# Optimization experiments

Measured on AMD Instinct MI355X. Metric: run time of the kernel, lower is better.

The kernel has to match this reference:

```python
import jax, jax.numpy as jnp
import numpy as np

B, V, S, H, I, L, NH = 32, 50, 64, 256, 512, 2, 4
VOCAB, SEGV, AGEV = 30000, 2, 144
EPS = 1e-12


def _ln(x, g, b):
    m = jnp.mean(x, axis=-1, keepdims=True)
    v = jnp.mean((x - m) ** 2, axis=-1, keepdims=True)
    return (x - m) / jnp.sqrt(v + EPS) * g + b


def _sinusoid_table(max_pos, hidden):
    pos = np.arange(max_pos, dtype=np.float32)[:, None]
    idx = np.arange(hidden, dtype=np.float32)[None, :]
    ang = pos / np.power(10000.0, 2.0 * idx / hidden)
    tab = np.where((np.arange(hidden) % 2 == 0)[None, :], np.sin(ang), np.cos(ang))
    return jnp.asarray(tab, dtype=jnp.float32)


def setup_inputs() -> dict:
    key = jax.random.key(0)
    ks = iter(jax.random.split(key, 48))

    def nrm(shape, s=0.02):
        return jax.random.normal(next(ks), shape, dtype=jnp.float32) * s

    inp = {
        "word": jax.random.randint(next(ks), (B, V, S), 0, VOCAB),
        "age": jax.random.randint(next(ks), (B, V, S), 0, AGEV),
        "seg": jax.random.randint(next(ks), (B, V, S), 0, SEGV),
        "posi": jax.random.randint(next(ks), (B, V, S), 0, S),
        "mask": jnp.ones((B, V, S), dtype=jnp.float32),
        "token": 0,
        "word_emb": nrm((VOCAB, H)),
        "seg_emb": nrm((SEGV, H)),
        "age_emb": nrm((AGEV, H)),
        "posi_emb": _sinusoid_table(S, H),
        "emb_ln_g": jnp.ones((H,), jnp.float32),
        "emb_ln_b": jnp.zeros((H,), jnp.float32),
        "qw": nrm((L, H, H)), "qb": jnp.zeros((L, H), jnp.float32),
        "kw": nrm((L, H, H)), "kb": jnp.zeros((L, H), jnp.float32),
        "vw": nrm((L, H, H)), "vb": jnp.zeros((L, H), jnp.float32),
        "ow": nrm((L, H, H)), "ob": jnp.zeros((L, H), jnp.float32),
        "attn_ln_g": jnp.ones((L, H), jnp.float32),
        "attn_ln_b": jnp.zeros((L, H), jnp.float32),
        "iw": nrm((L, H, I)), "ib": jnp.zeros((L, I), jnp.float32),
        "outw": nrm((L, I, H)), "outb": jnp.zeros((L, H), jnp.float32),
        "out_ln_g": jnp.ones((L, H), jnp.float32),
        "out_ln_b": jnp.zeros((L, H), jnp.float32),
        "pool_w": nrm((H, H)), "pool_b": jnp.zeros((H,), jnp.float32),
    }
    return inp


def reference(word, age, seg, posi, mask, token,
              word_emb, seg_emb, age_emb, posi_emb, emb_ln_g, emb_ln_b,
              qw, qb, kw, kb, vw, vb, ow, ob, attn_ln_g, attn_ln_b,
              iw, ib, outw, outb, out_ln_g, out_ln_b, pool_w, pool_b):
    # token embeddings: word + seg + age + sinusoidal position, then LayerNorm
    emb = word_emb[word] + seg_emb[seg] + age_emb[age] + posi_emb[posi]  # [B,V,S,H]
    x = _ln(emb, emb_ln_g, emb_ln_b)
    N = B * V
    x = x.reshape(N, S, H)  # vectorize the per-visit loop over the batch axis
    am = ((1.0 - mask) * -10000.0).reshape(N, 1, 1, S)  # additive attention mask
    d = H // NH
    scale = 1.0 / jnp.sqrt(jnp.float32(d))
    n_layers = qw.shape[0]
    for l in range(n_layers):
        q = (x @ qw[l] + qb[l]).reshape(N, S, NH, d)
        k = (x @ kw[l] + kb[l]).reshape(N, S, NH, d)
        v = (x @ vw[l] + vb[l]).reshape(N, S, NH, d)
        scores = jnp.einsum("bqhd,bkhd->bhqk", q, k) * scale + am
        probs = jax.nn.softmax(scores, axis=-1)  # dropout = identity (eval)
        ctx = jnp.einsum("bhqk,bkhd->bqhd", probs, v).reshape(N, S, H)
        a = _ln(ctx @ ow[l] + ob[l] + x, attn_ln_g[l], attn_ln_b[l])
        h = jax.nn.gelu(a @ iw[l] + ib[l], approximate=False)
        x = _ln(h @ outw[l] + outb[l] + a, out_ln_g[l], out_ln_b[l])
    first = x[:, 0].reshape(B, V, H)  # pooler with token=False: hidden[:, 0]
    return jnp.tanh(first @ pool_w + pool_b)  # [B, V, H]
```

## Files before the change

### kernel.cpp

```cpp
#include <hip/hip_runtime.h>
#include <math.h>

typedef __attribute__((ext_vector_type(8))) short short8;
typedef __attribute__((ext_vector_type(4))) short short4v;
typedef __attribute__((ext_vector_type(4))) float f32x4;

#define M_TOT 102400

__device__ __forceinline__ unsigned short f2b(float f) {
  unsigned u = __float_as_uint(f);
  return (unsigned short)((u + 0x7fffu + ((u >> 16) & 1u)) >> 16);
}
__device__ __forceinline__ float b2f(unsigned short h) {
  return __uint_as_float(((unsigned)h) << 16);
}
__device__ __forceinline__ f32x4 mfma16(short8 a, short8 b, f32x4 c) {
  return __builtin_amdgcn_mfma_f32_16x16x32_bf16(a, b, c, 0, 0, 0);
}
template <int STRIDE>
__device__ __forceinline__ short8 lds8(const short* buf, int row, int k) {
  int idx = (row * STRIDE + k) ^ ((row & 7) << 3);
  return *(const short8*)(buf + idx);
}
template <int STRIDE>
__device__ __forceinline__ void ldsw(short* buf, int row, int col, unsigned short v) {
  buf[(row * STRIDE + col) ^ ((row & 7) << 3)] = (short)v;
}
__device__ __forceinline__ float red16sum(float v) {
  v += __shfl_xor(v, 1); v += __shfl_xor(v, 2);
  v += __shfl_xor(v, 4); v += __shfl_xor(v, 8);
  return v;
}
__device__ __forceinline__ float red16max(float v) {
  v = fmaxf(v, __shfl_xor(v, 1)); v = fmaxf(v, __shfl_xor(v, 2));
  v = fmaxf(v, __shfl_xor(v, 4)); v = fmaxf(v, __shfl_xor(v, 8));
  return v;
}

__device__ __forceinline__ void stage16k(const short* __restrict__ g, short* l,
                                         int w, int lane) {
  const char* gb = (const char*)g + w * 4096 + lane * 16;
  char* lb = (char*)l + w * 4096;
#pragma unroll
  for (int c = 0; c < 4; ++c)
    __builtin_amdgcn_global_load_lds(
        (const __attribute__((address_space(1))) unsigned int*)(gb + c * 1024),
        (__attribute__((address_space(3))) unsigned int*)(lb + c * 1024), 16, 0, 0);
}

template <int KB>
__device__ __forceinline__ void gemm_core(const short* __restrict__ A, int lda,
                                          const short* __restrict__ Wimg,
                                          short* sB, f32x4 acc[16], int r0,
                                          int w, int lane, int l15, int g4) {
  short8 af[KB];
#pragma unroll
  for (int kk = 0; kk < KB; ++kk)
    af[kk] = *(const short8*)(A + (r0 + l15) * lda + kk * 32 + g4 * 8);
  stage16k(Wimg, sB, w, lane);
  __syncthreads();
#pragma unroll
  for (int kb = 0; kb < KB; ++kb) {
    if (kb + 1 < KB)
      stage16k(Wimg + (kb + 1) * 8192, sB + ((kb + 1) & 1) * 8192, w, lane);
    const short* cur = sB + (kb & 1) * 8192;
#pragma unroll
    for (int tc = 0; tc < 16; ++tc) {
      int row = tc * 16 + l15;
      short8 bf = *(const short8*)(cur + ((row * 32 + g4 * 8) ^ ((row & 7) << 3)));
      acc[tc] = mfma16(af[kb], bf, acc[tc]);
    }
    __syncthreads();
  }
}

__device__ __forceinline__ void ln_epi(f32x4 acc[16], short* x,
                                       const float* __restrict__ bias,
                                       const float* __restrict__ g_,
                                       const float* __restrict__ b_,
                                       int r0, int l15, int g4) {
  float s1[4] = {0.f, 0.f, 0.f, 0.f}, s2[4] = {0.f, 0.f, 0.f, 0.f};
#pragma unroll
  for (int tc = 0; tc < 16; ++tc) {
    int col = tc * 16 + l15;
    float bv = bias[col];
#pragma unroll
    for (int r = 0; r < 4; ++r) {
      float v = acc[tc][r] + bv + b2f((unsigned short)x[(r0 + g4 * 4 + r) * 256 + col]);
      acc[tc][r] = v;
      s1[r] += v; s2[r] += v * v;
    }
  }
  float mean[4], rstd[4];
#pragma unroll
  for (int r = 0; r < 4; ++r) {
    float a = red16sum(s1[r]), q = red16sum(s2[r]);
    mean[r] = a * (1.f / 256.f);
    rstd[r] = rsqrtf(q * (1.f / 256.f) - mean[r] * mean[r] + 1e-12f);
  }
#pragma unroll
  for (int tc = 0; tc < 16; ++tc) {
    int col = tc * 16 + l15;
    float gv = g_[col], bv = b_[col];
#pragma unroll
    for (int r = 0; r < 4; ++r)
      x[(r0 + g4 * 4 + r) * 256 + col] =
          (short)f2b((acc[tc][r] - mean[r]) * rstd[r] * gv + bv);
  }
}

__global__ void prep_w(const float* __restrict__ qw, const float* __restrict__ kw,
                       const float* __restrict__ vw, const float* __restrict__ ow,
                       const float* __restrict__ iw, const float* __restrict__ outw,
                       const float* __restrict__ pw, short* __restrict__ ws) {
  int t = blockIdx.x * 256 + threadIdx.x;
  float val; int base, n, k;
  if (t < 524288) {
    int which = t >> 17, r = t & 131071;
    int ly = r >> 16, e = r & 65535;
    n = e >> 8; k = e & 255;
    const float* m = which == 0 ? qw : which == 1 ? kw : which == 2 ? vw : ow;
    val = m[(ly * 256 + k) * 256 + n];
    base = which * 131072 + ly * 65536;
  } else if (t < 786432) {
    int e = t - 524288;
    int ly = e >> 17, f = e & 131071, g2 = f >> 16, e2 = f & 65535;
    n = e2 >> 8; k = e2 & 255;
    val = iw[(ly * 256 + k) * 512 + g2 * 256 + n];
    base = 524288 + ly * 131072 + g2 * 65536;
  } else if (t < 1048576) {
    int e = t - 786432;
    int ly = e >> 17, f = e & 131071;
    n = f >> 9; k = f & 511;
    val = outw[(ly * 512 + k) * 256 + n];
    base = 786432 + ly * 131072;
  } else {
    int e = t - 1048576;
    n = e >> 8; k = e & 255;
    val = pw[k * 256 + n];
    base = 1048576;
  }
  int pos = ((n * 32 + (k & 31)) ^ ((n & 7) << 3));
  ws[base + (k >> 5) * 8192 + pos] = (short)f2b(val);
}

__global__ __launch_bounds__(256) void emb_k(
    const int* __restrict__ word, const int* __restrict__ age,
    const int* __restrict__ seg, const int* __restrict__ posi,
    const float* __restrict__ we, const float* __restrict__ se,
    const float* __restrict__ ae, const float* __restrict__ pe,
    const float* __restrict__ g, const float* __restrict__ b,
    short* __restrict__ x) {
  int w = threadIdx.x >> 6, lane = threadIdx.x & 63;
  int t = blockIdx.x * 4 + w;
  int wi = word[t], gi = seg[t], ai = age[t], pi = posi[t];
  f32x4 e = ((const f32x4*)(we + wi * 256))[lane];
  f32x4 tv = ((const f32x4*)(se + gi * 256))[lane]; e = e + tv;
  tv = ((const f32x4*)(ae + ai * 256))[lane]; e = e + tv;
  tv = ((const f32x4*)(pe + pi * 256))[lane]; e = e + tv;
  float s1 = e[0] + e[1] + e[2] + e[3];
  float s2 = e[0] * e[0] + e[1] * e[1] + e[2] * e[2] + e[3] * e[3];
#pragma unroll
  for (int m = 1; m < 64; m <<= 1) { s1 += __shfl_xor(s1, m); s2 += __shfl_xor(s2, m); }
  float mean = s1 * (1.f / 256.f);
  float rstd = rsqrtf(s2 * (1.f / 256.f) - mean * mean + 1e-12f);
  f32x4 gv = ((const f32x4*)g)[lane];
  f32x4 bv = ((const f32x4*)b)[lane];
  short4v pk;
#pragma unroll
  for (int j = 0; j < 4; ++j) pk[j] = (short)f2b((e[j] - mean) * rstd * gv[j] + bv[j]);
  *(short4v*)(x + t * 256 + lane * 4) = pk;
}

__global__ __launch_bounds__(256) void qkv3_k(
    const short* __restrict__ x, const short* __restrict__ img,
    const float* __restrict__ qb_, const float* __restrict__ kb_,
    const float* __restrict__ vb_,
    short* __restrict__ q, short* __restrict__ k2, short* __restrict__ vt, int ly) {
  __shared__ __align__(16) short sB[16384];
  int w = threadIdx.x >> 6, lane = threadIdx.x & 63;
  int l15 = lane & 15, g4 = lane >> 4;
  int y = blockIdx.y;
  int r0 = blockIdx.x * 64 + w * 16;
  const short* W = img + y * 131072 + ly * 65536;
  const float* bias = (y == 0 ? qb_ : y == 1 ? kb_ : vb_) + ly * 256;
  f32x4 acc[16];
#pragma unroll
  for (int i = 0; i < 16; ++i) acc[i] = f32x4{0.f, 0.f, 0.f, 0.f};
  gemm_core<8>(x, 256, W, sB, acc, r0, w, lane, l15, g4);
  if (y < 2) {
    short* out = y ? k2 : q;
#pragma unroll
    for (int tc = 0; tc < 16; ++tc) {
      int col = tc * 16 + l15;
      float bv = bias[col];
#pragma unroll
      for (int r = 0; r < 4; ++r)
        out[(r0 + g4 * 4 + r) * 256 + col] = (short)f2b(acc[tc][r] + bv);
    }
  } else {
#pragma unroll
    for (int tc = 0; tc < 16; ++tc) {
      int col = tc * 16 + l15;
      float bv = bias[col];
#pragma unroll
      for (int r = 0; r < 4; ++r) {
        int tok = r0 + g4 * 4 + r;
        vt[(tok >> 6) * 16384 + col * 64 + (tok & 63)] = (short)f2b(acc[tc][r] + bv);
      }
    }
  }
}

__global__ __launch_bounds__(256) void attn_k(
    const short* __restrict__ q, const short* __restrict__ k,
    const short* __restrict__ vt, short* __restrict__ ctx,
    const float* __restrict__ mask) {
  __shared__ __align__(16) short sP[16384];
  int w = threadIdx.x >> 6, lane = threadIdx.x & 63;
  int l15 = lane & 15, g4 = lane >> 4;
  int n = blockIdx.x;
  const f32x4 zero4 = {0.f, 0.f, 0.f, 0.f};
  short* sPw = sP + w * 4096;

  float amvr[4];
#pragma unroll
  for (int tc = 0; tc < 4; ++tc)
    amvr[tc] = (1.f - mask[n * 64 + tc * 16 + l15]) * -10000.f;

  const short* qn = q + n * 16384;
  const short* kn = k + n * 16384;
  const short* vtn = vt + n * 16384;

  short8 qa[4][2];
#pragma unroll
  for (int st = 0; st < 4; ++st)
#pragma unroll
    for (int ks = 0; ks < 2; ++ks)
      qa[st][ks] = *(const short8*)(qn + (st * 16 + l15) * 256 + w * 64 + ks * 32 + g4 * 8);
  f32x4 sacc[4][4];
#pragma unroll
  for (int st = 0; st < 4; ++st)
#pragma unroll
    for (int tc = 0; tc < 4; ++tc) sacc[st][tc] = zero4;
#pragma unroll
  for (int ks = 0; ks < 2; ++ks)
#pragma unroll
    for (int tc = 0; tc < 4; ++tc) {
      short8 kf = *(const short8*)(kn + (tc * 16 + l15) * 256 + w * 64 + ks * 32 + g4 * 8);
#pragma unroll
      for (int st = 0; st < 4; ++st) sacc[st][tc] = mfma16(qa[st][ks], kf, sacc[st][tc]);
    }
#pragma unroll
  for (int st = 0; st < 4; ++st)
#pragma unroll
    for (int r = 0; r < 4; ++r) {
      float pv[4];
      float mx = -1e30f;
#pragma unroll
      for (int tc = 0; tc < 4; ++tc) {
        float sv = sacc[st][tc][r] * 0.125f + amvr[tc];
        pv[tc] = sv;
        mx = fmaxf(mx, sv);
      }
      mx = red16max(mx);
      float sm = 0.f;
#pragma unroll
      for (int tc = 0; tc < 4; ++tc) {
        float e = __expf(pv[tc] - mx);
        pv[tc] = e;
        sm += e;
      }
      sm = red16sum(sm);
      float inv = 1.f / sm;
#pragma unroll
      for (int tc = 0; tc < 4; ++tc)
        ldsw<64>(sPw, st * 16 + g4 * 4 + r, tc * 16 + l15, f2b(pv[tc] * inv));
    }
  __syncthreads();

  f32x4 cacc[4][4];
#pragma unroll
  for (int st = 0; st < 4; ++st)
#pragma unroll
    for (int tc = 0; tc < 4; ++tc) cacc[st][tc] = zero4;
#pragma unroll
  for (int ks = 0; ks < 2; ++ks) {
    short8 pa[4];
#pragma unroll
    for (int st = 0; st < 4; ++st) pa[st] = lds8<64>(sPw, st * 16 + l15, ks * 32 + g4 * 8);
#pragma unroll
    for (int tc = 0; tc < 4; ++tc) {
      short8 vf = *(const short8*)(vtn + (w * 64 + tc * 16 + l15) * 64 + ks * 32 + g4 * 8);
#pragma unroll
      for (int st = 0; st < 4; ++st) cacc[st][tc] = mfma16(pa[st], vf, cacc[st][tc]);
    }
  }
#pragma unroll
  for (int st = 0; st < 4; ++st)
#pragma unroll
    for (int tc = 0; tc < 4; ++tc)
#pragma unroll
      for (int r = 0; r < 4; ++r)
        ctx[(n * 64 + st * 16 + g4 * 4 + r) * 256 + w * 64 + tc * 16 + l15] =
            (short)f2b(cacc[st][tc][r]);
}

__global__ __launch_bounds__(256) void oln_k(
    const short* __restrict__ ctx, const short* __restrict__ img,
    const float* __restrict__ bias, short* __restrict__ x,
    const float* __restrict__ g_, const float* __restrict__ b_) {
  __shared__ __align__(16) short sB[16384];
  int w = threadIdx.x >> 6, lane = threadIdx.x & 63;
  int l15 = lane & 15, g4 = lane >> 4;
  int r0 = blockIdx.x * 64 + w * 16;
  f32x4 acc[16];
#pragma unroll
  for (int i = 0; i < 16; ++i) acc[i] = f32x4{0.f, 0.f, 0.f, 0.f};
  gemm_core<8>(ctx, 256, img, sB, acc, r0, w, lane, l15, g4);
  ln_epi(acc, x, bias, g_, b_, r0, l15, g4);
}

__global__ __launch_bounds__(256) void ffn1_k(
    const short* __restrict__ x, const short* __restrict__ img,
    const float* __restrict__ bias, short* __restrict__ h) {
  __shared__ __align__(16) short sB[16384];
  int w = threadIdx.x >> 6, lane = threadIdx.x & 63;
  int l15 = lane & 15, g4 = lane >> 4;
  int y = blockIdx.y;
  int r0 = blockIdx.x * 64 + w * 16;
  f32x4 acc[16];
#pragma unroll
  for (int i = 0; i < 16; ++i) acc[i] = f32x4{0.f, 0.f, 0.f, 0.f};
  gemm_core<8>(x, 256, img + y * 65536, sB, acc, r0, w, lane, l15, g4);
  const float* bs = bias + y * 256;
#pragma unroll
  for (int tc = 0; tc < 16; ++tc) {
    int col = tc * 16 + l15;
    float bv = bs[col];
#pragma unroll
    for (int r = 0; r < 4; ++r) {
      float v = acc[tc][r] + bv;
      v = 0.5f * v * (1.f + erff(v * 0.70710678118f));
      h[(r0 + g4 * 4 + r) * 512 + y * 256 + col] = (short)f2b(v);
    }
  }
}

__global__ __launch_bounds__(256) void ffn2_k(
    const short* __restrict__ h, const short* __restrict__ img,
    const float* __restrict__ bias, short* __restrict__ x,
    const float* __restrict__ g_, const float* __restrict__ b_) {
  __shared__ __align__(16) short sB[16384];
  int w = threadIdx.x >> 6, lane = threadIdx.x & 63;
  int l15 = lane & 15, g4 = lane >> 4;
  int r0 = blockIdx.x * 64 + w * 16;
  f32x4 acc[16];
#pragma unroll
  for (int i = 0; i < 16; ++i) acc[i] = f32x4{0.f, 0.f, 0.f, 0.f};
  gemm_core<16>(h, 512, img, sB, acc, r0, w, lane, l15, g4);
  ln_epi(acc, x, bias, g_, b_, r0, l15, g4);
}

__global__ __launch_bounds__(256) void pool_k(
    const short* __restrict__ x, const short* __restrict__ img,
    const float* __restrict__ pb, float* __restrict__ out) {
  __shared__ __align__(16) short sB[16384];
  int w = threadIdx.x >> 6, lane = threadIdx.x & 63;
  int l15 = lane & 15, g4 = lane >> 4;
  int r0 = blockIdx.x * 64 + w * 16;
  f32x4 acc[16];
#pragma unroll
  for (int i = 0; i < 16; ++i) acc[i] = f32x4{0.f, 0.f, 0.f, 0.f};
  gemm_core<8>(x, 16384, img, sB, acc, r0, w, lane, l15, g4);
#pragma unroll
  for (int tc = 0; tc < 16; ++tc) {
    int col = tc * 16 + l15;
    float bv = pb[col];
#pragma unroll
    for (int r = 0; r < 4; ++r)
      out[(r0 + g4 * 4 + r) * 256 + col] = tanhf(acc[tc][r] + bv);
  }
}

extern "C" void kernel_launch(void* const* d_in, const int* in_sizes, int n_in,
                              void* d_out, int out_size, void* d_ws, size_t ws_size,
                              hipStream_t stream) {
  const int* word = (const int*)d_in[0];
  const int* age = (const int*)d_in[1];
  const int* seg = (const int*)d_in[2];
  const int* posi = (const int*)d_in[3];
  const float* mask = (const float*)d_in[4];
  const float* word_emb = (const float*)d_in[6];
  const float* seg_emb = (const float*)d_in[7];
  const float* age_emb = (const float*)d_in[8];
  const float* posi_emb = (const float*)d_in[9];
  const float* emb_g = (const float*)d_in[10];
  const float* emb_b = (const float*)d_in[11];
  const float* qw = (const float*)d_in[12];
  const float* qb = (const float*)d_in[13];
  const float* kw = (const float*)d_in[14];
  const float* kb = (const float*)d_in[15];
  const float* vw = (const float*)d_in[16];
  const float* vb = (const float*)d_in[17];
  const float* ow = (const float*)d_in[18];
  const float* ob = (const float*)d_in[19];
  const float* attn_g = (const float*)d_in[20];
  const float* attn_b = (const float*)d_in[21];
  const float* iw = (const float*)d_in[22];
  const float* ib = (const float*)d_in[23];
  const float* outw = (const float*)d_in[24];
  const float* outb = (const float*)d_in[25];
  const float* out_g = (const float*)d_in[26];
  const float* out_b = (const float*)d_in[27];
  const float* pool_w = (const float*)d_in[28];
  const float* pool_b = (const float*)d_in[29];
  short* ws = (short*)d_ws;

  short* xb_ = ws + 1114112;
  short* qbuf = xb_ + 26214400;
  short* kbuf = qbuf + 26214400;
  short* vtbuf = kbuf + 26214400;
  short* hbuf = qbuf;

  prep_w<<<4352, 256, 0, stream>>>(qw, kw, vw, ow, iw, outw, pool_w, ws);
  emb_k<<<25600, 256, 0, stream>>>(word, age, seg, posi, word_emb, seg_emb,
                                   age_emb, posi_emb, emb_g, emb_b, xb_);
  for (int ly = 0; ly < 2; ++ly) {
    qkv3_k<<<dim3(1600, 3), 256, 0, stream>>>(xb_, ws, qb, kb, vb, qbuf, kbuf,
                                              vtbuf, ly);
    attn_k<<<1600, 256, 0, stream>>>(qbuf, kbuf, vtbuf, qbuf, mask);
    oln_k<<<1600, 256, 0, stream>>>(qbuf, ws + 393216 + ly * 65536, ob + ly * 256,
                                    xb_, attn_g + ly * 256, attn_b + ly * 256);
    ffn1_k<<<dim3(1600, 2), 256, 0, stream>>>(xb_, ws + 524288 + ly * 131072,
                                              ib + ly * 512, hbuf);
    ffn2_k<<<1600, 256, 0, stream>>>(hbuf, ws + 786432 + ly * 131072,
                                     outb + ly * 256, xb_, out_g + ly * 256,
                                     out_b + ly * 256);
  }
  pool_k<<<25, 256, 0, stream>>>(xb_, ws + 1048576, pool_b, (float*)d_out);
}
```

Measured before the change: 709.3 us.

## Fuse attention with output projection and retile GEMMs to 64x64 per wave

Each GEMM is retiled so every wave owns 64 output columns across all 64 rows, instead of 16 rows across all 256 columns. A-fragments are loaded once per block and reused across the Q/K/V and FFN1 output tiles, which replaces the extra grid dimension. The attention kernel now keeps the context in LDS and runs the output projection plus residual LayerNorm directly, so the ctx round-trip through global memory and one launch go away. The LayerNorm reduction now needs a cross-wave LDS partial-sum step with an extra barrier, and the larger af register arrays raise register pressure and may lower occupancy.

After: 1.186 ms. 67.2% more time.

```diff
diff --git a/kernel.cpp b/kernel.cpp
--- a/kernel.cpp
+++ b/kernel.cpp
@@ -4,8 +4,6 @@
 typedef __attribute__((ext_vector_type(8))) short short8;
 typedef __attribute__((ext_vector_type(4))) short short4v;
 typedef __attribute__((ext_vector_type(4))) float f32x4;
-
-#define M_TOT 102400
 
 __device__ __forceinline__ unsigned short f2b(float f) {
   unsigned u = __float_as_uint(f);
@@ -49,14 +47,10 @@
 }
 
 template <int KB>
-__device__ __forceinline__ void gemm_core(const short* __restrict__ A, int lda,
-                                          const short* __restrict__ Wimg,
-                                          short* sB, f32x4 acc[16], int r0,
-                                          int w, int lane, int l15, int g4) {
-  short8 af[KB];
-#pragma unroll
-  for (int kk = 0; kk < KB; ++kk)
-    af[kk] = *(const short8*)(A + (r0 + l15) * lda + kk * 32 + g4 * 8);
+__device__ __forceinline__ void gemm64(const short8 af[][4],
+                                       const short* __restrict__ Wimg,
+                                       short* sB, f32x4 acc[4][4],
+                                       int w, int lane, int l15, int g4) {
   stage16k(Wimg, sB, w, lane);
   __syncthreads();
 #pragma unroll
@@ -65,47 +59,74 @@
       stage16k(Wimg + (kb + 1) * 8192, sB + ((kb + 1) & 1) * 8192, w, lane);
     const short* cur = sB + (kb & 1) * 8192;
 #pragma unroll
-    for (int tc = 0; tc < 16; ++tc) {
-      int row = tc * 16 + l15;
-      short8 bf = *(const short8*)(cur + ((row * 32 + g4 * 8) ^ ((row & 7) << 3)));
-      acc[tc] = mfma16(af[kb], bf, acc[tc]);
+    for (int tc = 0; tc < 4; ++tc) {
+      int n = w * 64 + tc * 16 + l15;
+      short8 bf = *(const short8*)(cur + ((n * 32 + g4 * 8) ^ ((n & 7) << 3)));
+#pragma unroll
+      for (int st = 0; st < 4; ++st)
+        acc[st][tc] = mfma16(af[kb][st], bf, acc[st][tc]);
     }
     __syncthreads();
   }
 }
 
-__device__ __forceinline__ void ln_epi(f32x4 acc[16], short* x,
-                                       const float* __restrict__ bias,
-                                       const float* __restrict__ g_,
-                                       const float* __restrict__ b_,
-                                       int r0, int l15, int g4) {
-  float s1[4] = {0.f, 0.f, 0.f, 0.f}, s2[4] = {0.f, 0.f, 0.f, 0.f};
-#pragma unroll
-  for (int tc = 0; tc < 16; ++tc) {
-    int col = tc * 16 + l15;
+__device__ __forceinline__ void ln_epi64(f32x4 acc[4][4], short* x,
+                                         const float* __restrict__ bias,
+                                         const float* __restrict__ g_,
+                                         const float* __restrict__ b_,
+                                         float (*part)[64][4],
+                                         int r0, int w, int l15, int g4) {
+  float s1[4][4], s2[4][4];
+#pragma unroll
+  for (int st = 0; st < 4; ++st)
+#pragma unroll
+    for (int r = 0; r < 4; ++r) { s1[st][r] = 0.f; s2[st][r] = 0.f; }
+#pragma unroll
+  for (int tc = 0; tc < 4; ++tc) {
+    int col = w * 64 + tc * 16 + l15;
     float bv = bias[col];
 #pragma unroll
+    for (int st = 0; st < 4; ++st)
+#pragma unroll
+      for (int r = 0; r < 4; ++r) {
+        float v = acc[st][tc][r] + bv +
+                  b2f((unsigned short)x[(r0 + st * 16 + g4 * 4 + r) * 256 + col]);
+        acc[st][tc][r] = v;
+        s1[st][r] += v; s2[st][r] += v * v;
+      }
+  }
+#pragma unroll
+  for (int st = 0; st < 4; ++st)
+#pragma unroll
     for (int r = 0; r < 4; ++r) {
-      float v = acc[tc][r] + bv + b2f((unsigned short)x[(r0 + g4 * 4 + r) * 256 + col]);
-      acc[tc][r] = v;
-      s1[r] += v; s2[r] += v * v;
-    }
-  }
-  float mean[4], rstd[4];
-#pragma unroll
-  for (int r = 0; r < 4; ++r) {
-    float a = red16sum(s1[r]), q = red16sum(s2[r]);
-    mean[r] = a * (1.f / 256.f);
-    rstd[r] = rsqrtf(q * (1.f / 256.f) - mean[r] * mean[r] + 1e-12f);
-  }
-#pragma unroll
-  for (int tc = 0; tc < 16; ++tc) {
-    int col = tc * 16 + l15;
+      float a = red16sum(s1[st][r]), q = red16sum(s2[st][r]);
+      if (l15 == 0) {
+        part[0][st * 16 + g4 * 4 + r][w] = a;
+        part[1][st * 16 + g4 * 4 + r][w] = q;
+      }
+    }
+  __syncthreads();
+#pragma unroll
+  for (int st = 0; st < 4; ++st)
+#pragma unroll
+    for (int r = 0; r < 4; ++r) {
+      int row = st * 16 + g4 * 4 + r;
+      float a = part[0][row][0] + part[0][row][1] + part[0][row][2] + part[0][row][3];
+      float q = part[1][row][0] + part[1][row][1] + part[1][row][2] + part[1][row][3];
+      float mean = a * (1.f / 256.f);
+      float rstd = rsqrtf(q * (1.f / 256.f) - mean * mean + 1e-12f);
+      s1[st][r] = mean; s2[st][r] = rstd;
+    }
+#pragma unroll
+  for (int tc = 0; tc < 4; ++tc) {
+    int col = w * 64 + tc * 16 + l15;
     float gv = g_[col], bv = b_[col];
 #pragma unroll
-    for (int r = 0; r < 4; ++r)
-      x[(r0 + g4 * 4 + r) * 256 + col] =
-          (short)f2b((acc[tc][r] - mean[r]) * rstd[r] * gv + bv);
+    for (int st = 0; st < 4; ++st)
+#pragma unroll
+      for (int r = 0; r < 4; ++r)
+        x[(r0 + st * 16 + g4 * 4 + r) * 256 + col] =
+            (short)f2b((acc[st][tc][r] - s1[st][r]) * s2[st][r] * gv + bv);
   }
 }
 
@@ -172,7 +193,7 @@
   *(short4v*)(x + t * 256 + lane * 4) = pk;
 }
 
-__global__ __launch_bounds__(256) void qkv3_k(
+__global__ __launch_bounds__(256) void qkv_k(
     const short* __restrict__ x, const short* __restrict__ img,
     const float* __restrict__ qb_, const float* __restrict__ kb_,
     const float* __restrict__ vb_,
@@ -180,48 +201,64 @@
   __shared__ __align__(16) short sB[16384];
   int w = threadIdx.x >> 6, lane = threadIdx.x & 63;
   int l15 = lane & 15, g4 = lane >> 4;
-  int y = blockIdx.y;
-  int r0 = blockIdx.x * 64 + w * 16;
-  const short* W = img + y * 131072 + ly * 65536;
-  const float* bias = (y == 0 ? qb_ : y == 1 ? kb_ : vb_) + ly * 256;
-  f32x4 acc[16];
-#pragma unroll
-  for (int i = 0; i < 16; ++i) acc[i] = f32x4{0.f, 0.f, 0.f, 0.f};
-  gemm_core<8>(x, 256, W, sB, acc, r0, w, lane, l15, g4);
-  if (y < 2) {
-    short* out = y ? k2 : q;
-#pragma unroll
-    for (int tc = 0; tc < 16; ++tc) {
-      int col = tc * 16 + l15;
-      float bv = bias[col];
-#pragma unroll
-      for (int r = 0; r < 4; ++r)
-        out[(r0 + g4 * 4 + r) * 256 + col] = (short)f2b(acc[tc][r] + bv);
-    }
-  } else {
-#pragma unroll
-    for (int tc = 0; tc < 16; ++tc) {
-      int col = tc * 16 + l15;
-      float bv = bias[col];
-#pragma unroll
-      for (int r = 0; r < 4; ++r) {
-        int tok = r0 + g4 * 4 + r;
-        vt[(tok >> 6) * 16384 + col * 64 + (tok & 63)] = (short)f2b(acc[tc][r] + bv);
+  int n = blockIdx.x;
+  int r0 = n * 64;
+  short8 af[8][4];
+#pragma unroll
+  for (int kk = 0; kk < 8; ++kk)
+#pragma unroll
+    for (int st = 0; st < 4; ++st)
+      af[kk][st] = *(const short8*)(x + (r0 + st * 16 + l15) * 256 + kk * 32 + g4 * 8);
+
+  for (int y = 0; y < 3; ++y) {
+    f32x4 acc[4][4];
+#pragma unroll
+    for (int st = 0; st < 4; ++st)
+#pragma unroll
+      for (int tc = 0; tc < 4; ++tc) acc[st][tc] = f32x4{0.f, 0.f, 0.f, 0.f};
+    gemm64<8>(af, img + y * 131072 + ly * 65536, sB, acc, w, lane, l15, g4);
+    const float* bias = (y == 0 ? qb_ : y == 1 ? kb_ : vb_) + ly * 256;
+    if (y < 2) {
+      short* out = y ? k2 : q;
+#pragma unroll
+      for (int tc = 0; tc < 4; ++tc) {
+        int col = w * 64 + tc * 16 + l15;
+        float bv = bias[col];
+#pragma unroll
+        for (int st = 0; st < 4; ++st)
+#pragma unroll
+          for (int r = 0; r < 4; ++r)
+            out[(r0 + st * 16 + g4 * 4 + r) * 256 + col] = (short)f2b(acc[st][tc][r] + bv);
       }
-    }
-  }
-}
-
-__global__ __launch_bounds__(256) void attn_k(
+    } else {
+#pragma unroll
+      for (int tc = 0; tc < 4; ++tc) {
+        int col = w * 64 + tc * 16 + l15;
+        float bv = bias[col];
+#pragma unroll
+        for (int st = 0; st < 4; ++st)
+#pragma unroll
+          for (int r = 0; r < 4; ++r)
+            vt[n * 16384 + col * 64 + st * 16 + g4 * 4 + r] = (short)f2b(acc[st][tc][r] + bv);
+      }
+    }
+  }
+}
+
+__global__ __launch_bounds__(256) void attnoln_k(
     const short* __restrict__ q, const short* __restrict__ k,
-    const short* __restrict__ vt, short* __restrict__ ctx,
+    const short* __restrict__ vt, const short* __restrict__ img,
+    const float* __restrict__ ob_, short* __restrict__ x,
+    const float* __restrict__ g_, const float* __restrict__ b_,
     const float* __restrict__ mask) {
-  __shared__ __align__(16) short sP[16384];
+  __shared__ __align__(16) short sCtx[16384];
+  __shared__ __align__(16) short sPB[16384];
+  __shared__ float part[2][64][4];
   int w = threadIdx.x >> 6, lane = threadIdx.x & 63;
   int l15 = lane & 15, g4 = lane >> 4;
   int n = blockIdx.x;
   const f32x4 zero4 = {0.f, 0.f, 0.f, 0.f};
-  short* sPw = sP + w * 4096;
+  short* sPw = sPB + w * 4096;
 
   float amvr[4];
 #pragma unroll
@@ -302,23 +339,23 @@
     for (int tc = 0; tc < 4; ++tc)
 #pragma unroll
       for (int r = 0; r < 4; ++r)
-        ctx[(n * 64 + st * 16 + g4 * 4 + r) * 256 + w * 64 + tc * 16 + l15] =
-            (short)f2b(cacc[st][tc][r]);
-}
-
-__global__ __launch_bounds__(256) void oln_k(
-    const short* __restrict__ ctx, const short* __restrict__ img,
-    const float* __restrict__ bias, short* __restrict__ x,
-    const float* __restrict__ g_, const float* __restrict__ b_) {
-  __shared__ __align__(16) short sB[16384];
-  int w = threadIdx.x >> 6, lane = threadIdx.x & 63;
-  int l15 = lane & 15, g4 = lane >> 4;
-  int r0 = blockIdx.x * 64 + w * 16;
-  f32x4 acc[16];
-#pragma unroll
-  for (int i = 0; i < 16; ++i) acc[i] = f32x4{0.f, 0.f, 0.f, 0.f};
-  gemm_core<8>(ctx, 256, img, sB, acc, r0, w, lane, l15, g4);
-  ln_epi(acc, x, bias, g_, b_, r0, l15, g4);
+        ldsw<256>(sCtx, st * 16 + g4 * 4 + r, w * 64 + tc * 16 + l15,
+                  f2b(cacc[st][tc][r]));
+  __syncthreads();
+
+  short8 af[8][4];
+#pragma unroll
+  for (int kk = 0; kk < 8; ++kk)
+#pragma unroll
+    for (int st = 0; st < 4; ++st)
+      af[kk][st] = lds8<256>(sCtx, st * 16 + l15, kk * 32 + g4 * 8);
+  f32x4 acc[4][4];
+#pragma unroll
+  for (int st = 0; st < 4; ++st)
+#pragma unroll
+    for (int tc = 0; tc < 4; ++tc) acc[st][tc] = zero4;
+  gemm64<8>(af, img, sPB, acc, w, lane, l15, g4);
+  ln_epi64(acc, x, ob_, g_, b_, part, n * 64, w, l15, g4);
 }
 
 __global__ __launch_bounds__(256) void ffn1_k(
@@ -327,22 +364,33 @@
   __shared__ __align__(16) short sB[16384];
   int w = threadIdx.x >> 6, lane = threadIdx.x & 63;
   int l15 = lane & 15, g4 = lane >> 4;
-  int y = blockIdx.y;
-  int r0 = blockIdx.x * 64 + w * 16;
-  f32x4 acc[16];
-#pragma unroll
-  for (int i = 0; i < 16; ++i) acc[i] = f32x4{0.f, 0.f, 0.f, 0.f};
-  gemm_core<8>(x, 256, img + y * 65536, sB, acc, r0, w, lane, l15, g4);
-  const float* bs = bias + y * 256;
-#pragma unroll
-  for (int tc = 0; tc < 16; ++tc) {
-    int col = tc * 16 + l15;
-    float bv = bs[col];
-#pragma unroll
-    for (int r = 0; r < 4; ++r) {
-      float v = acc[tc][r] + bv;
-      v = 0.5f * v * (1.f + erff(v * 0.70710678118f));
-      h[(r0 + g4 * 4 + r) * 512 + y * 256 + col] = (short)f2b(v);
+  int r0 = blockIdx.x * 64;
+  short8 af[8][4];
+#pragma unroll
+  for (int kk = 0; kk < 8; ++kk)
+#pragma unroll
+    for (int st = 0; st < 4; ++st)
+      af[kk][st] = *(const short8*)(x + (r0 + st * 16 + l15) * 256 + kk * 32 + g4 * 8);
+  for (int p = 0; p < 2; ++p) {
+    f32x4 acc[4][4];
+#pragma unroll
+    for (int st = 0; st < 4; ++st)
+#pragma unroll
+      for (int tc = 0; tc < 4; ++tc) acc[st][tc] = f32x4{0.f, 0.f, 0.f, 0.f};
+    gemm64<8>(af, img + p * 65536, sB, acc, w, lane, l15, g4);
+    const float* bs = bias + p * 256;
+#pragma unroll
+    for (int tc = 0; tc < 4; ++tc) {
+      int col = w * 64 + tc * 16 + l15;
+      float bv = bs[col];
+#pragma unroll
+      for (int st = 0; st < 4; ++st)
+#pragma unroll
+        for (int r = 0; r < 4; ++r) {
+          float v = acc[st][tc][r] + bv;
+          v = 0.5f * v * (1.f + erff(v * 0.70710678118f));
+          h[(r0 + st * 16 + g4 * 4 + r) * 512 + p * 256 + col] = (short)f2b(v);
+        }
     }
   }
 }
@@ -352,14 +400,26 @@
     const float* __restrict__ bias, short* __restrict__ x,
     const float* __restrict__ g_, const float* __restrict__ b_) {
   __shared__ __align__(16) short sB[16384];
+  __shared__ float part[2][64][4];
   int w = threadIdx.x >> 6, lane = threadIdx.x & 63;
   int l15 = lane & 15, g4 = lane >> 4;
-  int r0 = blockIdx.x * 64 + w * 16;
-  f32x4 acc[16];
-#pragma unroll
-  for (int i = 0; i < 16; ++i) acc[i] = f32x4{0.f, 0.f, 0.f, 0.f};
-  gemm_core<16>(h, 512, img, sB, acc, r0, w, lane, l15, g4);
-  ln_epi(acc, x, bias, g_, b_, r0, l15, g4);
+  int r0 = blockIdx.x * 64;
+  f32x4 acc[4][4];
+#pragma unroll
+  for (int st = 0; st < 4; ++st)
+#pragma unroll
+    for (int tc = 0; tc < 4; ++tc) acc[st][tc] = f32x4{0.f, 0.f, 0.f, 0.f};
+  for (int half = 0; half < 2; ++half) {
+    short8 af[8][4];
+#pragma unroll
+    for (int kk = 0; kk < 8; ++kk)
+#pragma unroll
+      for (int st = 0; st < 4; ++st)
+        af[kk][st] = *(const short8*)(h + (r0 + st * 16 + l15) * 512 + half * 256 +
+                                      kk * 32 + g4 * 8);
+    gemm64<8>(af, img + half * 65536, sB, acc, w, lane, l15, g4);
+  }
+  ln_epi64(acc, x, bias, g_, b_, part, r0, w, l15, g4);
 }
 
 __global__ __launch_bounds__(256) void pool_k(
@@ -368,18 +428,29 @@
   __shared__ __align__(16) short sB[16384];
   int w = threadIdx.x >> 6, lane = threadIdx.x & 63;
   int l15 = lane & 15, g4 = lane >> 4;
-  int r0 = blockIdx.x * 64 + w * 16;
-  f32x4 acc[16];
-#pragma unroll
-  for (int i = 0; i < 16; ++i) acc[i] = f32x4{0.f, 0.f, 0.f, 0.f};
-  gemm_core<8>(x, 16384, img, sB, acc, r0, w, lane, l15, g4);
-#pragma unroll
-  for (int tc = 0; tc < 16; ++tc) {
-    int col = tc * 16 + l15;
+  int r0 = blockIdx.x * 64;
+  short8 af[8][4];
+#pragma unroll
+  for (int kk = 0; kk < 8; ++kk)
+#pragma unroll
+    for (int st = 0; st < 4; ++st)
+      af[kk][st] = *(const short8*)(x + (size_t)(r0 + st * 16 + l15) * 16384 +
+                                    kk * 32 + g4 * 8);
+  f32x4 acc[4][4];
+#pragma unroll
+  for (int st = 0; st < 4; ++st)
+#pragma unroll
+    for (int tc = 0; tc < 4; ++tc) acc[st][tc] = f32x4{0.f, 0.f, 0.f, 0.f};
+  gemm64<8>(af, img, sB, acc, w, lane, l15, g4);
+#pragma unroll
+  for (int tc = 0; tc < 4; ++tc) {
+    int col = w * 64 + tc * 16 + l15;
     float bv = pb[col];
 #pragma unroll
-    for (int r = 0; r < 4; ++r)
-      out[(r0 + g4 * 4 + r) * 256 + col] = tanhf(acc[tc][r] + bv);
+    for (int st = 0; st < 4; ++st)
+#pragma unroll
+      for (int r = 0; r < 4; ++r)
+        out[(r0 + st * 16 + g4 * 4 + r) * 256 + col] = tanhf(acc[st][tc][r] + bv);
   }
 }
 
@@ -427,13 +498,12 @@
   emb_k<<<25600, 256, 0, stream>>>(word, age, seg, posi, word_emb, seg_emb,
                                    age_emb, posi_emb, emb_g, emb_b, xb_);
   for (int ly = 0; ly < 2; ++ly) {
-    qkv3_k<<<dim3(1600, 3), 256, 0, stream>>>(xb_, ws, qb, kb, vb, qbuf, kbuf,
-                                              vtbuf, ly);
-    attn_k<<<1600, 256, 0, stream>>>(qbuf, kbuf, vtbuf, qbuf, mask);
-    oln_k<<<1600, 256, 0, stream>>>(qbuf, ws + 393216 + ly * 65536, ob + ly * 256,
-                                    xb_, attn_g + ly * 256, attn_b + ly * 256);
-    ffn1_k<<<dim3(1600, 2), 256, 0, stream>>>(xb_, ws + 524288 + ly * 131072,
-                                              ib + ly * 512, hbuf);
+    qkv_k<<<1600, 256, 0, stream>>>(xb_, ws, qb, kb, vb, qbuf, kbuf, vtbuf, ly);
+    attnoln_k<<<1600, 256, 0, stream>>>(qbuf, kbuf, vtbuf, ws + 393216 + ly * 65536,
+                                        ob + ly * 256, xb_, attn_g + ly * 256,
+                                        attn_b + ly * 256, mask);
+    ffn1_k<<<1600, 256, 0, stream>>>(xb_, ws + 524288 + ly * 131072, ib + ly * 512,
+                                     hbuf);
     ffn2_k<<<1600, 256, 0, stream>>>(hbuf, ws + 786432 + ly * 131072,
                                      outb + ly * 256, xb_, out_g + ly * 256,
                                      out_b + ly * 256);
```

## Retile GEMM warps to 2x2 layout and use tanh-approx GELU

Applied to the files above, without the earlier changes.

Each warp now computes a 32x128 output tile, so every LDS B fragment is reused across two row subtiles. This halves the LDS reads per MFMA compared with the old 16x256 per-warp tile. LayerNorm epilogues now reduce row statistics across two warps through a shared partial-sum buffer and an extra barrier. FFN2 is split into two K halves to bound register use. GELU switches from erf to a sigmoid-form tanh approximation with a fast exp, which trades some accuracy for fewer instructions.

After: 903.6 us. 27.4% more time.

```diff
diff --git a/kernel.cpp b/kernel.cpp
--- a/kernel.cpp
+++ b/kernel.cpp
@@ -4,8 +4,6 @@
 typedef __attribute__((ext_vector_type(8))) short short8;
 typedef __attribute__((ext_vector_type(4))) short short4v;
 typedef __attribute__((ext_vector_type(4))) float f32x4;
-
-#define M_TOT 102400
 
 __device__ __forceinline__ unsigned short f2b(float f) {
   unsigned u = __float_as_uint(f);
@@ -49,14 +47,10 @@
 }
 
 template <int KB>
-__device__ __forceinline__ void gemm_core(const short* __restrict__ A, int lda,
+__device__ __forceinline__ void gemm_core(const short8 af[][2],
                                           const short* __restrict__ Wimg,
-                                          short* sB, f32x4 acc[16], int r0,
+                                          short* sB, f32x4 acc[2][8],
                                           int w, int lane, int l15, int g4) {
-  short8 af[KB];
-#pragma unroll
-  for (int kk = 0; kk < KB; ++kk)
-    af[kk] = *(const short8*)(A + (r0 + l15) * lda + kk * 32 + g4 * 8);
   stage16k(Wimg, sB, w, lane);
   __syncthreads();
 #pragma unroll
@@ -65,47 +59,75 @@
       stage16k(Wimg + (kb + 1) * 8192, sB + ((kb + 1) & 1) * 8192, w, lane);
     const short* cur = sB + (kb & 1) * 8192;
 #pragma unroll
-    for (int tc = 0; tc < 16; ++tc) {
-      int row = tc * 16 + l15;
-      short8 bf = *(const short8*)(cur + ((row * 32 + g4 * 8) ^ ((row & 7) << 3)));
-      acc[tc] = mfma16(af[kb], bf, acc[tc]);
+    for (int tc = 0; tc < 8; ++tc) {
+      int n = (w & 1) * 128 + tc * 16 + l15;
+      short8 bf = *(const short8*)(cur + ((n * 32 + g4 * 8) ^ ((n & 7) << 3)));
+#pragma unroll
+      for (int st = 0; st < 2; ++st)
+        acc[st][tc] = mfma16(af[kb][st], bf, acc[st][tc]);
     }
     __syncthreads();
   }
 }
 
-__device__ __forceinline__ void ln_epi(f32x4 acc[16], short* x,
+__device__ __forceinline__ void ln_epi(f32x4 acc[2][8], short* x,
                                        const float* __restrict__ bias,
                                        const float* __restrict__ g_,
                                        const float* __restrict__ b_,
-                                       int r0, int l15, int g4) {
-  float s1[4] = {0.f, 0.f, 0.f, 0.f}, s2[4] = {0.f, 0.f, 0.f, 0.f};
-#pragma unroll
-  for (int tc = 0; tc < 16; ++tc) {
-    int col = tc * 16 + l15;
+                                       float (*part)[64][2],
+                                       int r0, int wr, int wc, int w,
+                                       int l15, int g4) {
+  float s1[2][4], s2[2][4];
+#pragma unroll
+  for (int st = 0; st < 2; ++st)
+#pragma unroll
+    for (int r = 0; r < 4; ++r) { s1[st][r] = 0.f; s2[st][r] = 0.f; }
+#pragma unroll
+  for (int tc = 0; tc < 8; ++tc) {
+    int col = wc + tc * 16 + l15;
     float bv = bias[col];
 #pragma unroll
+    for (int st = 0; st < 2; ++st)
+#pragma unroll
+      for (int r = 0; r < 4; ++r) {
+        float v = acc[st][tc][r] + bv +
+                  b2f((unsigned short)x[(r0 + wr + st * 16 + g4 * 4 + r) * 256 + col]);
+        acc[st][tc][r] = v;
+        s1[st][r] += v; s2[st][r] += v * v;
+      }
+  }
+#pragma unroll
+  for (int st = 0; st < 2; ++st)
+#pragma unroll
     for (int r = 0; r < 4; ++r) {
-      float v = acc[tc][r] + bv + b2f((unsigned short)x[(r0 + g4 * 4 + r) * 256 + col]);
-      acc[tc][r] = v;
-      s1[r] += v; s2[r] += v * v;
-    }
-  }
-  float mean[4], rstd[4];
-#pragma unroll
-  for (int r = 0; r < 4; ++r) {
-    float a = red16sum(s1[r]), q = red16sum(s2[r]);
-    mean[r] = a * (1.f / 256.f);
-    rstd[r] = rsqrtf(q * (1.f / 256.f) - mean[r] * mean[r] + 1e-12f);
-  }
-#pragma unroll
-  for (int tc = 0; tc < 16; ++tc) {
-    int col = tc * 16 + l15;
+      float a = red16sum(s1[st][r]), q = red16sum(s2[st][r]);
+      if (l15 == 0) {
+        part[0][wr + st * 16 + g4 * 4 + r][w & 1] = a;
+        part[1][wr + st * 16 + g4 * 4 + r][w & 1] = q;
+      }
+    }
+  __syncthreads();
+#pragma unroll
+  for (int st = 0; st < 2; ++st)
+#pragma unroll
+    for (int r = 0; r < 4; ++r) {
+      int row = wr + st * 16 + g4 * 4 + r;
+      float a = part[0][row][0] + part[0][row][1];
+      float q = part[1][row][0] + part[1][row][1];
+      float mean = a * (1.f / 256.f);
+      float rstd = rsqrtf(q * (1.f / 256.f) - mean * mean + 1e-12f);
+      s1[st][r] = mean; s2[st][r] = rstd;
+    }
+#pragma unroll
+  for (int tc = 0; tc < 8; ++tc) {
+    int col = wc + tc * 16 + l15;
     float gv = g_[col], bv = b_[col];
 #pragma unroll
-    for (int r = 0; r < 4; ++r)
-      x[(r0 + g4 * 4 + r) * 256 + col] =
-          (short)f2b((acc[tc][r] - mean[r]) * rstd[r] * gv + bv);
+    for (int st = 0; st < 2; ++st)
+#pragma unroll
+      for (int r = 0; r < 4; ++r)
+        x[(r0 + wr + st * 16 + g4 * 4 + r) * 256 + col] =
+            (short)f2b((acc[st][tc][r] - s1[st][r]) * s2[st][r] * gv + bv);
   }
 }
 
@@ -180,34 +202,48 @@
   __shared__ __align__(16) short sB[16384];
   int w = threadIdx.x >> 6, lane = threadIdx.x & 63;
   int l15 = lane & 15, g4 = lane >> 4;
+  int wr = (w >> 1) * 32, wc = (w & 1) * 128;
   int y = blockIdx.y;
-  int r0 = blockIdx.x * 64 + w * 16;
+  int n = blockIdx.x;
+  int r0 = n * 64;
   const short* W = img + y * 131072 + ly * 65536;
   const float* bias = (y == 0 ? qb_ : y == 1 ? kb_ : vb_) + ly * 256;
-  f32x4 acc[16];
-#pragma unroll
-  for (int i = 0; i < 16; ++i) acc[i] = f32x4{0.f, 0.f, 0.f, 0.f};
-  gemm_core<8>(x, 256, W, sB, acc, r0, w, lane, l15, g4);
+  short8 af[8][2];
+#pragma unroll
+  for (int kk = 0; kk < 8; ++kk)
+#pragma unroll
+    for (int st = 0; st < 2; ++st)
+      af[kk][st] = *(const short8*)(x + (r0 + wr + st * 16 + l15) * 256 + kk * 32 + g4 * 8);
+  f32x4 acc[2][8];
+#pragma unroll
+  for (int st = 0; st < 2; ++st)
+#pragma unroll
+    for (int tc = 0; tc < 8; ++tc) acc[st][tc] = f32x4{0.f, 0.f, 0.f, 0.f};
+  gemm_core<8>(af, W, sB, acc, w, lane, l15, g4);
   if (y < 2) {
     short* out = y ? k2 : q;
 #pragma unroll
-    for (int tc = 0; tc < 16; ++tc) {
-      int col = tc * 16 + l15;
+    for (int tc = 0; tc < 8; ++tc) {
+      int col = wc + tc * 16 + l15;
       float bv = bias[col];
 #pragma unroll
-      for (int r = 0; r < 4; ++r)
-        out[(r0 + g4 * 4 + r) * 256 + col] = (short)f2b(acc[tc][r] + bv);
+      for (int st = 0; st < 2; ++st)
+#pragma unroll
+        for (int r = 0; r < 4; ++r)
+          out[(r0 + wr + st * 16 + g4 * 4 + r) * 256 + col] =
+              (short)f2b(acc[st][tc][r] + bv);
     }
   } else {
 #pragma unroll
-    for (int tc = 0; tc < 16; ++tc) {
-      int col = tc * 16 + l15;
+    for (int tc = 0; tc < 8; ++tc) {
+      int col = wc + tc * 16 + l15;
       float bv = bias[col];
 #pragma unroll
-      for (int r = 0; r < 4; ++r) {
-        int tok = r0 + g4 * 4 + r;
-        vt[(tok >> 6) * 16384 + col * 64 + (tok & 63)] = (short)f2b(acc[tc][r] + bv);
-      }
+      for (int st = 0; st < 2; ++st)
+#pragma unroll
+        for (int r = 0; r < 4; ++r)
+          vt[n * 16384 + col * 64 + wr + st * 16 + g4 * 4 + r] =
+              (short)f2b(acc[st][tc][r] + bv);
     }
   }
 }
@@ -311,14 +347,24 @@
     const float* __restrict__ bias, short* __restrict__ x,
     const float* __restrict__ g_, const float* __restrict__ b_) {
   __shared__ __align__(16) short sB[16384];
+  __shared__ float part[2][64][2];
   int w = threadIdx.x >> 6, lane = threadIdx.x & 63;
   int l15 = lane & 15, g4 = lane >> 4;
-  int r0 = blockIdx.x * 64 + w * 16;
-  f32x4 acc[16];
-#pragma unroll
-  for (int i = 0; i < 16; ++i) acc[i] = f32x4{0.f, 0.f, 0.f, 0.f};
-  gemm_core<8>(ctx, 256, img, sB, acc, r0, w, lane, l15, g4);
-  ln_epi(acc, x, bias, g_, b_, r0, l15, g4);
+  int wr = (w >> 1) * 32, wc = (w & 1) * 128;
+  int r0 = blockIdx.x * 64;
+  short8 af[8][2];
+#pragma unroll
+  for (int kk = 0; kk < 8; ++kk)
+#pragma unroll
+    for (int st = 0; st < 2; ++st)
+      af[kk][st] = *(const short8*)(ctx + (r0 + wr + st * 16 + l15) * 256 + kk * 32 + g4 * 8);
+  f32x4 acc[2][8];
+#pragma unroll
+  for (int st = 0; st < 2; ++st)
+#pragma unroll
+    for (int tc = 0; tc < 8; ++tc) acc[st][tc] = f32x4{0.f, 0.f, 0.f, 0.f};
+  gemm_core<8>(af, img, sB, acc, w, lane, l15, g4);
+  ln_epi(acc, x, bias, g_, b_, part, r0, wr, wc, w, l15, g4);
 }
 
 __global__ __launch_bounds__(256) void ffn1_k(
@@ -327,23 +373,35 @@
   __shared__ __align__(16) short sB[16384];
   int w = threadIdx.x >> 6, lane = threadIdx.x & 63;
   int l15 = lane & 15, g4 = lane >> 4;
+  int wr = (w >> 1) * 32, wc = (w & 1) * 128;
   int y = blockIdx.y;
-  int r0 = blockIdx.x * 64 + w * 16;
-  f32x4 acc[16];
-#pragma unroll
-  for (int i = 0; i < 16; ++i) acc[i] = f32x4{0.f, 0.f, 0.f, 0.f};
-  gemm_core<8>(x, 256, img + y * 65536, sB, acc, r0, w, lane, l15, g4);
+  int r0 = blockIdx.x * 64;
+  short8 af[8][2];
+#pragma unroll
+  for (int kk = 0; kk < 8; ++kk)
+#pragma unroll
+    for (int st = 0; st < 2; ++st)
+      af[kk][st] = *(const short8*)(x + (r0 + wr + st * 16 + l15) * 256 + kk * 32 + g4 * 8);
+  f32x4 acc[2][8];
+#pragma unroll
+  for (int st = 0; st < 2; ++st)
+#pragma unroll
+    for (int tc = 0; tc < 8; ++tc) acc[st][tc] = f32x4{0.f, 0.f, 0.f, 0.f};
+  gemm_core<8>(af, img + y * 65536, sB, acc, w, lane, l15, g4);
   const float* bs = bias + y * 256;
 #pragma unroll
-  for (int tc = 0; tc < 16; ++tc) {
-    int col = tc * 16 + l15;
+  for (int tc = 0; tc < 8; ++tc) {
+    int col = wc + tc * 16 + l15;
     float bv = bs[col];
 #pragma unroll
-    for (int r = 0; r < 4; ++r) {
-      float v = acc[tc][r] + bv;
-      v = 0.5f * v * (1.f + erff(v * 0.70710678118f));
-      h[(r0 + g4 * 4 + r) * 512 + y * 256 + col] = (short)f2b(v);
-    }
+    for (int st = 0; st < 2; ++st)
+#pragma unroll
+      for (int r = 0; r < 4; ++r) {
+        float v = acc[st][tc][r] + bv;
+        float z = 1.5957691f * (v + 0.044715f * v * v * v);
+        v = v / (1.f + __expf(-z));
+        h[(r0 + wr + st * 16 + g4 * 4 + r) * 512 + y * 256 + col] = (short)f2b(v);
+      }
   }
 }
 
@@ -352,14 +410,27 @@
     const float* __restrict__ bias, short* __restrict__ x,
     const float* __restrict__ g_, const float* __restrict__ b_) {
   __shared__ __align__(16) short sB[16384];
+  __shared__ float part[2][64][2];
   int w = threadIdx.x >> 6, lane = threadIdx.x & 63;
   int l15 = lane & 15, g4 = lane >> 4;
-  int r0 = blockIdx.x * 64 + w * 16;
-  f32x4 acc[16];
-#pragma unroll
-  for (int i = 0; i < 16; ++i) acc[i] = f32x4{0.f, 0.f, 0.f, 0.f};
-  gemm_core<16>(h, 512, img, sB, acc, r0, w, lane, l15, g4);
-  ln_epi(acc, x, bias, g_, b_, r0, l15, g4);
+  int wr = (w >> 1) * 32, wc = (w & 1) * 128;
+  int r0 = blockIdx.x * 64;
+  f32x4 acc[2][8];
+#pragma unroll
+  for (int st = 0; st < 2; ++st)
+#pragma unroll
+    for (int tc = 0; tc < 8; ++tc) acc[st][tc] = f32x4{0.f, 0.f, 0.f, 0.f};
+  for (int half = 0; half < 2; ++half) {
+    short8 af[8][2];
+#pragma unroll
+    for (int kk = 0; kk < 8; ++kk)
+#pragma unroll
+      for (int st = 0; st < 2; ++st)
+        af[kk][st] = *(const short8*)(h + (r0 + wr + st * 16 + l15) * 512 + half * 256 +
+                                      kk * 32 + g4 * 8);
+    gemm_core<8>(af, img + half * 65536, sB, acc, w, lane, l15, g4);
+  }
+  ln_epi(acc, x, bias, g_, b_, part, r0, wr, wc, w, l15, g4);
 }
 
 __global__ __launch_bounds__(256) void pool_k(
@@ -368,18 +439,30 @@
   __shared__ __align__(16) short sB[16384];
   int w = threadIdx.x >> 6, lane = threadIdx.x & 63;
   int l15 = lane & 15, g4 = lane >> 4;
-  int r0 = blockIdx.x * 64 + w * 16;
-  f32x4 acc[16];
-#pragma unroll
-  for (int i = 0; i < 16; ++i) acc[i] = f32x4{0.f, 0.f, 0.f, 0.f};
-  gemm_core<8>(x, 16384, img, sB, acc, r0, w, lane, l15, g4);
-#pragma unroll
-  for (int tc = 0; tc < 16; ++tc) {
-    int col = tc * 16 + l15;
+  int wr = (w >> 1) * 32, wc = (w & 1) * 128;
+  int r0 = blockIdx.x * 64;
+  short8 af[8][2];
+#pragma unroll
+  for (int kk = 0; kk < 8; ++kk)
+#pragma unroll
+    for (int st = 0; st < 2; ++st)
+      af[kk][st] = *(const short8*)(x + (size_t)(r0 + wr + st * 16 + l15) * 16384 +
+                                    kk * 32 + g4 * 8);
+  f32x4 acc[2][8];
+#pragma unroll
+  for (int st = 0; st < 2; ++st)
+#pragma unroll
+    for (int tc = 0; tc < 8; ++tc) acc[st][tc] = f32x4{0.f, 0.f, 0.f, 0.f};
+  gemm_core<8>(af, img, sB, acc, w, lane, l15, g4);
+#pragma unroll
+  for (int tc = 0; tc < 8; ++tc) {
+    int col = wc + tc * 16 + l15;
     float bv = pb[col];
 #pragma unroll
-    for (int r = 0; r < 4; ++r)
-      out[(r0 + g4 * 4 + r) * 256 + col] = tanhf(acc[tc][r] + bv);
+    for (int st = 0; st < 2; ++st)
+#pragma unroll
+      for (int r = 0; r < 4; ++r)
+        out[(r0 + wr + st * 16 + g4 * 4 + r) * 256 + col] = tanhf(acc[st][tc][r] + bv);
   }
 }
 
```
